# Performance work log

Measured on AMD Instinct MI355X. Metric: run time of the kernel, lower is better.

## Reference

```python
import jax, jax.numpy as jnp
import numpy as np

B, T, H, C, R = 8, 8192, 128, 128, 128  # batch, points, hidden, c_dim, plane reso
EPS = 1e-3  # 10e-4 in original
PLANE_COLS = ((0, 2), (0, 1), (1, 2))  # xz, xy, yz


def _normalize_coordinate(p, cols):
    # normalize_coordinate with padding=0.0: p in [-0.5,0.5] -> [0,1), clipped
    xy = p[..., jnp.array(cols)] / (1.0 + 0.0 + EPS) + 0.5
    return jnp.clip(xy, 0.0, 1.0 - EPS)


def _coordinate2index(xy):
    g = jnp.floor(xy * R).astype(jnp.int32)  # [B,T,2]
    return g[..., 0] + R * g[..., 1]  # [B,T]


def _resblock(x, w0, b0, w1, b1, ws):
    # ResnetBlockFC: fc_1(relu(fc_0(relu(x)))) + shortcut(x)
    net = jax.nn.relu(x) @ w0 + b0
    dx = jax.nn.relu(net) @ w1 + b1
    return x @ ws + dx


def _pool_local(c, idx_list):
    # c: [B,T,F]; scatter_max into R*R bins per plane, gather back, sum over planes
    def one(cb, ib):  # cb [T,F], ib [T]
        out = jnp.full((R * R, cb.shape[-1]), -jnp.inf, cb.dtype).at[ib].max(cb)
        out = jnp.where(jnp.isinf(out), jnp.zeros_like(out), out)  # empty bins -> 0
        return out[ib]  # gather-broadcast back to points
    pooled = jnp.zeros_like(c)
    for idx in idx_list:
        pooled = pooled + jax.vmap(one)(c, idx)
    return pooled


def _plane_features(cfeat, idx):
    # scatter_mean of [B,T,C] into [B, C, R, R]
    def one(cb, ib):  # cb [T,C], ib [T]
        sums = jnp.zeros((R * R, cb.shape[-1]), cb.dtype).at[ib].add(cb)
        cnt = jnp.zeros((R * R,), cb.dtype).at[ib].add(1.0)
        return sums / jnp.clip(cnt, 1.0, None)[:, None]
    m = jax.vmap(one)(cfeat, idx)  # [B, R*R, C]
    return m.transpose(0, 2, 1).reshape(cfeat.shape[0], cfeat.shape[-1], R, R)


def _forward(p, p2, wp, bp, wp2, bp2,
             blk_w0, blk_b0, blk_w1, blk_b1, blk_ws,
             blkc_w0, blkc_b0, blkc_w1, blkc_b1, blkc_ws,
             fc_c_w, fc_c_b, fc_cc_w, fc_cc_b):
    idx_list = [_coordinate2index(_normalize_coordinate(p, cols)) for cols in PLANE_COLS]

    # feat_pos (PointNetPlusPlusAttnFusion) surrogate: per-point projections + additive fusion
    net = p @ wp + bp                  # [B,T,2H] geometry stream
    net_corr = net + (p2 @ wp2 + bp2)  # [B,T,2H] fused articulation stream

    net = _resblock(net, blk_w0[0], blk_b0[0], blk_w1[0], blk_b1[0], blk_ws[0])
    for i in range(1, blk_w0.shape[0]):
        pooled = _pool_local(net, idx_list)
        net = _resblock(jnp.concatenate([net, pooled], axis=-1),
                        blk_w0[i], blk_b0[i], blk_w1[i], blk_b1[i], blk_ws[i])
    c = net @ fc_c_w + fc_c_b  # [B,T,C]

    net_corr = _resblock(net_corr, blkc_w0[0], blkc_b0[0], blkc_w1[0], blkc_b1[0], blkc_ws[0])
    for i in range(1, blkc_w0.shape[0]):
        pooled = _pool_local(net_corr, idx_list)
        net_corr = _resblock(jnp.concatenate([net_corr, pooled], axis=-1),
                             blkc_w0[i], blkc_b0[i], blkc_w1[i], blkc_b1[i], blkc_ws[i])
    c_corr = net_corr @ fc_cc_w + fc_cc_b  # [B,T,C]

    planes = [_plane_features(c, idx) for idx in idx_list]
    planes += [_plane_features(c_corr, idx) for idx in idx_list]
    # order: geo_xz, geo_xy, geo_yz, corr_xz, corr_xy, corr_yz
    return jnp.stack(planes)  # [6, B, C, R, R]


def setup_inputs() -> dict:
    key = jax.random.key(0)
    ks = jax.random.split(key, 24)
    s = 0.05
    def n(i, shape):
        return jax.random.normal(ks[i], shape, jnp.float32) * s
    NB = 5
    return {
        "p": jax.random.uniform(ks[0], (B, T, 3), jnp.float32, -0.5, 0.5),
        "p2": jax.random.uniform(ks[1], (B, T, 3), jnp.float32, -0.5, 0.5),
        "wp": n(2, (3, 2 * H)), "bp": jnp.zeros((2 * H,), jnp.float32),
        "wp2": n(3, (3, 2 * H)), "bp2": jnp.zeros((2 * H,), jnp.float32),
        "blk_w0": n(4, (NB, 2 * H, H)), "blk_b0": jnp.zeros((NB, H), jnp.float32),
        "blk_w1": n(5, (NB, H, H)), "blk_b1": jnp.zeros((NB, H), jnp.float32),
        "blk_ws": n(6, (NB, 2 * H, H)),
        "blkc_w0": n(7, (NB, 2 * H, H)), "blkc_b0": jnp.zeros((NB, H), jnp.float32),
        "blkc_w1": n(8, (NB, H, H)), "blkc_b1": jnp.zeros((NB, H), jnp.float32),
        "blkc_ws": n(9, (NB, 2 * H, H)),
        "fc_c_w": n(10, (H, C)), "fc_c_b": jnp.zeros((C,), jnp.float32),
        "fc_cc_w": n(11, (H, C)), "fc_cc_b": jnp.zeros((C,), jnp.float32),
    }


def reference(p, p2, wp, bp, wp2, bp2,
              blk_w0, blk_b0, blk_w1, blk_b1, blk_ws,
              blkc_w0, blkc_b0, blkc_w1, blkc_b1, blkc_ws,
              fc_c_w, fc_c_b, fc_cc_w, fc_cc_b):
    return _forward(p, p2, wp, bp, wp2, bp2,
                    blk_w0, blk_b0, blk_w1, blk_b1, blk_ws,
                    blkc_w0, blkc_b0, blkc_w1, blkc_b1, blkc_ws,
                    fc_c_w, fc_c_b, fc_cc_w, fc_cc_b)
```

## Files before the change

### kernel.cpp

```cpp
#include <hip/hip_runtime.h>
#include <cstdint>
#include <cstddef>

#define Bn 8
#define Tn 8192
#define BT (Bn*Tn)
#define Hn 128
#define RRn 16384

typedef unsigned short u16;
typedef __attribute__((ext_vector_type(8))) short s8v;
typedef __attribute__((ext_vector_type(4))) float f4v;

#define SSTR ((size_t)BT*128)

__device__ __forceinline__ u16 f2bf(float f) {
  unsigned u = __float_as_uint(f);
  unsigned r = (u + 0x7FFF + ((u >> 16) & 1)) >> 16;
  return (u16)r;
}
__device__ __forceinline__ unsigned pack2(float a, float b) {
  return (unsigned)f2bf(a) | ((unsigned)f2bf(b) << 16);
}

__device__ __forceinline__ s8v relu8(s8v a) {
  union { s8v s; unsigned u[4]; } x; x.s = a;
#pragma unroll
  for (int k = 0; k < 4; ++k) {
    unsigned m = ((x.u[k] & 0x80008000u) >> 15) * 0xFFFFu;
    x.u[k] &= ~m;
  }
  return x.s;
}

__device__ __forceinline__ void upk(unsigned u, float& lo, float& hi) {
  lo = __uint_as_float(u << 16);
  hi = __uint_as_float(u & 0xFFFF0000u);
}

__global__ void k_idx(const float* __restrict__ p, int* __restrict__ idx,
                      int* __restrict__ cnt32) {
  int i = blockIdx.x*256 + threadIdx.x;
  if (i >= BT) return;
  int b = i >> 13;
  float v0 = p[i*3+0], v1 = p[i*3+1], v2 = p[i*3+2];
  float v[3] = {v0, v1, v2};
  const int A0[3] = {0,0,1};
  const int A1[3] = {2,1,2};
#pragma unroll
  for (int pl = 0; pl < 3; ++pl) {
    float a = v[A0[pl]] / 1.001f + 0.5f;
    float bq = v[A1[pl]] / 1.001f + 0.5f;
    a = fminf(fmaxf(a, 0.0f), 0.999f);
    bq = fminf(fmaxf(bq, 0.0f), 0.999f);
    int ga = (int)floorf(a * 128.0f);
    int gb = (int)floorf(bq * 128.0f);
    int bin = ga + 128*gb;
    idx[pl*BT + i] = bin;
    atomicAdd(&cnt32[(pl*Bn + b)*RRn + bin], 1);
  }
}

__global__ void k_scan(const int* __restrict__ cnt32, int* __restrict__ starts,
                       int* __restrict__ cursor) {
  int seg = blockIdx.x;
  const int* c = cnt32 + seg*RRn;
  int* st = starts + seg*RRn;
  int* cu = cursor + seg*RRn;
  int t = threadIdx.x;
  __shared__ int part[256];
  int base = t*64;
  int sum = 0;
#pragma unroll 8
  for (int j = 0; j < 64; ++j) sum += c[base+j];
  part[t] = sum; __syncthreads();
  for (int ofs = 1; ofs < 256; ofs <<= 1) {
    int v = (t >= ofs) ? part[t-ofs] : 0;
    __syncthreads();
    part[t] += v;
    __syncthreads();
  }
  int run = (t ? part[t-1] : 0) + seg*Tn;
#pragma unroll 8
  for (int j = 0; j < 64; ++j) { st[base+j] = run; cu[base+j] = run; run += c[base+j]; }
}

__global__ void k_fill(const int* __restrict__ idx, int* __restrict__ cursor,
                       int* __restrict__ sorted) {
  int g = blockIdx.x*256 + threadIdx.x;
  if (g >= 3*BT) return;
  int pl = g >> 16, i = g & (BT-1);
  int b = i >> 13;
  int pos = atomicAdd(&cursor[(pl*Bn + b)*RRn + idx[g]], 1);
  sorted[pos] = i;
}

__global__ void k_prep(const float* __restrict__ bw0, const float* __restrict__ bw1,
                       const float* __restrict__ bws, const float* __restrict__ cw0,
                       const float* __restrict__ cw1, const float* __restrict__ cws,
                       const float* __restrict__ fcw, const float* __restrict__ fccw,
                       u16* __restrict__ arena) {
  int c = blockIdx.x;
  int s = c / 26, r = c % 26;
  const float* base;
  if (r < 10)      base = (s ? cw0 : bw0) + (size_t)(r >> 1)*32768 + (size_t)(r & 1)*16384;
  else if (r < 15) base = (s ? cw1 : bw1) + (size_t)(r - 10)*16384;
  else if (r < 25) base = (s ? cws : bws) + (size_t)((r - 15) >> 1)*32768 + (size_t)((r - 15) & 1)*16384;
  else             base = s ? fccw : fcw;
  __shared__ u16 ld[128*130];
#pragma unroll 4
  for (int it = 0; it < 64; ++it) {
    int lin = it*256 + threadIdx.x;
    int k = lin >> 7, n = lin & 127;
    ld[k*130 + n] = f2bf(base[lin]);
  }
  __syncthreads();
  u16* dst = arena + (size_t)c*16384;
#pragma unroll 4
  for (int it = 0; it < 64; ++it) {
    int lin = it*256 + threadIdx.x;
    int n = lin >> 7, k = lin & 127;
    dst[lin] = ld[k*130 + n];
  }
}

template<int MODE>
__global__ __launch_bounds__(512, 2) void k_rb(
    const u16* __restrict__ xAb, const u16* __restrict__ xBb,
    const float* __restrict__ p, const float* __restrict__ p2,
    const float* __restrict__ wp, const float* __restrict__ bp,
    const float* __restrict__ wp2, const float* __restrict__ bp2,
    const u16* __restrict__ arena,
    int cw00, int cw01, int cws0, int cws1, int cw1c, int cfcw,
    const float* __restrict__ b0g, const float* __restrict__ b0c,
    const float* __restrict__ b1g, const float* __restrict__ b1c,
    const float* __restrict__ fcbg, const float* __restrict__ fcbc,
    u16* __restrict__ outb)
{
  const int y = blockIdx.y;
  const u16* ar = arena + (size_t)y*26*16384;
  const u16* w00 = ar + (size_t)cw00*16384;
  const u16* w01 = ar + (size_t)cw01*16384;
  const u16* ws0 = ar + (size_t)cws0*16384;
  const u16* ws1 = ar + (size_t)cws1*16384;
  const u16* w1c = ar + (size_t)cw1c*16384;
  const u16* fcw = ar + (size_t)cfcw*16384;
  const float* b0 = y ? b0c : b0g;
  const float* b1 = y ? b1c : b1g;
  const float* fcb = y ? fcbc : fcbg;
  const u16* xA = xAb + (size_t)y*SSTR;
  const u16* xB = xBb + (size_t)y*SSTR;
  u16* outp = outb + (size_t)y*SSTR;

  __shared__ u16 xs [256*72];
  __shared__ u16 w0s[128*72];
  __shared__ u16 wss[128*72];
  __shared__ u16 hid[256*136];
  const int tid = threadIdx.x;
  const size_t row0 = (size_t)blockIdx.x * 256;
  const int l = tid & 63, w = tid >> 6;
  const int lm = l & 15, lg = l >> 4;
  const int trow = tid >> 1, th = tid & 1;
  const int wn = tid >> 2, wq = tid & 3;

  f4v acc_h[2][8], acc_s[2][8];
#pragma unroll
  for (int mi = 0; mi < 2; ++mi)
#pragma unroll
    for (int j = 0; j < 8; ++j) { acc_h[mi][j] = (f4v){0,0,0,0}; acc_s[mi][j] = (f4v){0,0,0,0}; }

  float pa0=0.f, pa1=0.f, pa2=0.f, pq0=0.f, pq1=0.f, pq2=0.f;
  if (MODE == 1) {
    int rr = (int)row0 + trow;
    pa0 = p[rr*3+0]; pa1 = p[rr*3+1]; pa2 = p[rr*3+2];
    if (y) { pq0 = p2[rr*3+0]; pq1 = p2[rr*3+1]; pq2 = p2[rr*3+2]; }
  }

  uint4 px0, px1, px2, px3, pwa, pwb, psa, psb;
  if (MODE != 1) {
    const uint4* s = (const uint4*)(xA + (row0 + trow)*128 + th*32);
    px0 = s[0]; px1 = s[1]; px2 = s[2]; px3 = s[3];
  }
  {
    const uint4* sw = (const uint4*)(w00 + wn*128 + wq*16);
    pwa = sw[0]; pwb = sw[1];
    const uint4* ss = (const uint4*)(ws0 + wn*128 + wq*16);
    psa = ss[0]; psb = ss[1];
  }

#pragma unroll 1
  for (int kc = 0; kc < 4; ++kc) {
    if (MODE == 1) {
      const int c0 = kc*64 + th*32;
      unsigned t16[16];
#pragma unroll
      for (int q = 0; q < 8; ++q) {
        int c = c0 + q*4;
        float4 w0v = *(const float4*)(wp + c);
        float4 w1v = *(const float4*)(wp + 256 + c);
        float4 w2v = *(const float4*)(wp + 512 + c);
        float4 bbv = *(const float4*)(bp + c);
        float v0 = pa0*w0v.x + pa1*w1v.x + pa2*w2v.x + bbv.x;
        float v1 = pa0*w0v.y + pa1*w1v.y + pa2*w2v.y + bbv.y;
        float v2 = pa0*w0v.z + pa1*w1v.z + pa2*w2v.z + bbv.z;
        float v3 = pa0*w0v.w + pa1*w1v.w + pa2*w2v.w + bbv.w;
        if (y) {
          float4 u0 = *(const float4*)(wp2 + c);
          float4 u1 = *(const float4*)(wp2 + 256 + c);
          float4 u2 = *(const float4*)(wp2 + 512 + c);
          float4 b2 = *(const float4*)(bp2 + c);
          v0 += pq0*u0.x + pq1*u1.x + pq2*u2.x + b2.x;
          v1 += pq0*u0.y + pq1*u1.y + pq2*u2.y + b2.y;
          v2 += pq0*u0.z + pq1*u1.z + pq2*u2.z + b2.z;
          v3 += pq0*u0.w + pq1*u1.w + pq2*u2.w + b2.w;
        }
        t16[q*2]   = pack2(v0, v1);
        t16[q*2+1] = pack2(v2, v3);
      }
      uint4* d = (uint4*)(xs + trow*72 + th*32);
      d[0] = make_uint4(t16[0], t16[1], t16[2], t16[3]);
      d[1] = make_uint4(t16[4], t16[5], t16[6], t16[7]);
      d[2] = make_uint4(t16[8], t16[9], t16[10], t16[11]);
      d[3] = make_uint4(t16[12], t16[13], t16[14], t16[15]);
    } else {
      uint4* d = (uint4*)(xs + trow*72 + th*32);
      d[0] = px0; d[1] = px1; d[2] = px2; d[3] = px3;
    }
    { uint4* d = (uint4*)(w0s + wn*72 + wq*16); d[0] = pwa; d[1] = pwb; }
    { uint4* d = (uint4*)(wss + wn*72 + wq*16); d[0] = psa; d[1] = psb; }
    __syncthreads();
    if (kc < 3) {
      const int kn = kc + 1;
      const int k0n = (kn & 1) * 64;
      if (MODE != 1) {
        const u16* xsrcn = (kn < 2) ? xA : xB;
        const uint4* s = (const uint4*)(xsrcn + (row0 + trow)*128 + k0n + th*32);
        px0 = s[0]; px1 = s[1]; px2 = s[2]; px3 = s[3];
      }
      const u16* w0srcn = (kn < 2) ? w00 : w01;
      const u16* wssrcn = (kn < 2) ? ws0 : ws1;
      const uint4* sw = (const uint4*)(w0srcn + wn*128 + k0n + wq*16);
      pwa = sw[0]; pwb = sw[1];
      const uint4* ss = (const uint4*)(wssrcn + wn*128 + k0n + wq*16);
      psa = ss[0]; psb = ss[1];
    }
#pragma unroll
    for (int kk = 0; kk < 2; ++kk) {
      const int ko = lg*8 + kk*32;
      s8v a0 = *(const s8v*)(xs + (w*32 + lm)*72 + ko);
      s8v a1 = *(const s8v*)(xs + (w*32 + 16 + lm)*72 + ko);
      s8v a0r = relu8(a0), a1r = relu8(a1);
#pragma unroll
      for (int nj = 0; nj < 8; ++nj) {
        s8v bh = *(const s8v*)(w0s + (nj*16 + lm)*72 + ko);
        acc_h[0][nj] = __builtin_amdgcn_mfma_f32_16x16x32_bf16(a0r, bh, acc_h[0][nj], 0, 0, 0);
        acc_h[1][nj] = __builtin_amdgcn_mfma_f32_16x16x32_bf16(a1r, bh, acc_h[1][nj], 0, 0, 0);
      }
#pragma unroll
      for (int nj = 0; nj < 8; ++nj) {
        s8v bs = *(const s8v*)(wss + (nj*16 + lm)*72 + ko);
        acc_s[0][nj] = __builtin_amdgcn_mfma_f32_16x16x32_bf16(a0, bs, acc_s[0][nj], 0, 0, 0);
        acc_s[1][nj] = __builtin_amdgcn_mfma_f32_16x16x32_bf16(a1, bs, acc_s[1][nj], 0, 0, 0);
      }
    }
    __syncthreads();
  }
  {
    const uint4* s1 = (const uint4*)(w1c + wn*128 + wq*16);
    uint4 aa = s1[0], bb2 = s1[1];
    const uint4* s2 = (const uint4*)(w1c + wn*128 + 64 + wq*16);
    uint4 cc = s2[0], dd = s2[1];
    { uint4* d = (uint4*)(w0s + wn*72 + wq*16); d[0] = aa; d[1] = bb2; }
    { uint4* d = (uint4*)(wss + wn*72 + wq*16); d[0] = cc; d[1] = dd; }
#pragma unroll
    for (int mi = 0; mi < 2; ++mi)
#pragma unroll
      for (int nj = 0; nj < 8; ++nj) {
        const int col = nj*16 + lm;
        const float bv = b0[col];
#pragma unroll
        for (int r = 0; r < 4; ++r) {
          int row = w*32 + mi*16 + lg*4 + r;
          hid[row*136 + col] = f2bf(fmaxf(acc_h[mi][nj][r] + bv, 0.0f));
        }
      }
  }
  __syncthreads();
#pragma unroll
  for (int kk = 0; kk < 4; ++kk) {
    const int koA = lg*8 + kk*32;
    const int koB = lg*8 + (kk & 1)*32;
    const u16* pb = (kk < 2) ? w0s : wss;
    s8v a0 = *(const s8v*)(hid + (w*32 + lm)*136 + koA);
    s8v a1 = *(const s8v*)(hid + (w*32 + 16 + lm)*136 + koA);
#pragma unroll
    for (int nj = 0; nj < 8; ++nj) {
      s8v bb = *(const s8v*)(pb + (nj*16 + lm)*72 + koB);
      acc_s[0][nj] = __builtin_amdgcn_mfma_f32_16x16x32_bf16(a0, bb, acc_s[0][nj], 0, 0, 0);
      acc_s[1][nj] = __builtin_amdgcn_mfma_f32_16x16x32_bf16(a1, bb, acc_s[1][nj], 0, 0, 0);
    }
  }
  if (MODE != 2) {
#pragma unroll
    for (int mi = 0; mi < 2; ++mi)
#pragma unroll
      for (int nj = 0; nj < 8; ++nj) {
        const int col = nj*16 + lm;
        const float bv = b1[col];
#pragma unroll
        for (int r = 0; r < 4; ++r) {
          int row = w*32 + mi*16 + lg*4 + r;
          outp[(row0 + row)*128 + col] = f2bf(acc_s[mi][nj][r] + bv);
        }
      }
  } else {
    __syncthreads();
    {
      const uint4* s1 = (const uint4*)(fcw + wn*128 + wq*16);
      uint4 aa = s1[0], bb2 = s1[1];
      const uint4* s2 = (const uint4*)(fcw + wn*128 + 64 + wq*16);
      uint4 cc = s2[0], dd = s2[1];
      { uint4* d = (uint4*)(w0s + wn*72 + wq*16); d[0] = aa; d[1] = bb2; }
      { uint4* d = (uint4*)(wss + wn*72 + wq*16); d[0] = cc; d[1] = dd; }
#pragma unroll
      for (int mi = 0; mi < 2; ++mi)
#pragma unroll
        for (int nj = 0; nj < 8; ++nj) {
          const int col = nj*16 + lm;
          const float bv = b1[col];
#pragma unroll
          for (int r = 0; r < 4; ++r) {
            int row = w*32 + mi*16 + lg*4 + r;
            hid[row*136 + col] = f2bf(acc_s[mi][nj][r] + bv);
          }
        }
    }
    __syncthreads();
    f4v accf[2][8];
#pragma unroll
    for (int mi = 0; mi < 2; ++mi)
#pragma unroll
      for (int j = 0; j < 8; ++j) accf[mi][j] = (f4v){0,0,0,0};
#pragma unroll
    for (int kk = 0; kk < 4; ++kk) {
      const int koA = lg*8 + kk*32;
      const int koB = lg*8 + (kk & 1)*32;
      const u16* pb = (kk < 2) ? w0s : wss;
      s8v a0 = *(const s8v*)(hid + (w*32 + lm)*136 + koA);
      s8v a1 = *(const s8v*)(hid + (w*32 + 16 + lm)*136 + koA);
#pragma unroll
      for (int nj = 0; nj < 8; ++nj) {
        s8v bb = *(const s8v*)(pb + (nj*16 + lm)*72 + koB);
        accf[0][nj] = __builtin_amdgcn_mfma_f32_16x16x32_bf16(a0, bb, accf[0][nj], 0, 0, 0);
        accf[1][nj] = __builtin_amdgcn_mfma_f32_16x16x32_bf16(a1, bb, accf[1][nj], 0, 0, 0);
      }
    }
#pragma unroll
    for (int mi = 0; mi < 2; ++mi)
#pragma unroll
      for (int nj = 0; nj < 8; ++nj) {
        const int col = nj*16 + lm;
        const float bv = fcb[col];
#pragma unroll
        for (int r = 0; r < 4; ++r) {
          int row = w*32 + mi*16 + lg*4 + r;
          outp[(row0 + row)*128 + col] = f2bf(accf[mi][nj][r] + bv);
        }
      }
  }
}

__global__ void k_pool(const int* __restrict__ idx, const int* __restrict__ starts,
                       const int* __restrict__ cnt32, const int* __restrict__ sorted,
                       const u16* __restrict__ netb, u16* __restrict__ pooledb) {
  const u16* net = netb + (size_t)blockIdx.y*SSTR;
  u16* pooled = pooledb + (size_t)blockIdx.y*SSTR;
  int g = blockIdx.x*256 + threadIdx.x;
  int sl = g & 15;
  int i = g >> 4;
  if (i >= BT) return;
  int b = i >> 13;
  float acc[8];
#pragma unroll
  for (int k = 0; k < 8; ++k) acc[k] = 0.0f;
#pragma unroll
  for (int pl = 0; pl < 3; ++pl) {
    int seg = (pl*Bn + b)*RRn + idx[pl*BT + i];
    int s = starts[seg];
    int e = s + cnt32[seg];
    float mx[8];
#pragma unroll
    for (int k = 0; k < 8; ++k) mx[k] = -3.0e38f;
    for (int j = s; j < e; ++j) {
      int jj = sorted[j];
      uint4 v = *(const uint4*)(net + (size_t)jj*128 + sl*8);
      float lo, hi;
      upk(v.x, lo, hi); mx[0] = fmaxf(mx[0], lo); mx[1] = fmaxf(mx[1], hi);
      upk(v.y, lo, hi); mx[2] = fmaxf(mx[2], lo); mx[3] = fmaxf(mx[3], hi);
      upk(v.z, lo, hi); mx[4] = fmaxf(mx[4], lo); mx[5] = fmaxf(mx[5], hi);
      upk(v.w, lo, hi); mx[6] = fmaxf(mx[6], lo); mx[7] = fmaxf(mx[7], hi);
    }
#pragma unroll
    for (int k = 0; k < 8; ++k) acc[k] += mx[k];
  }
  union { uint4 v; unsigned u[4]; } o;
#pragma unroll
  for (int k = 0; k < 4; ++k)
    o.u[k] = (unsigned)f2bf(acc[2*k]) | ((unsigned)f2bf(acc[2*k+1]) << 16);
  *(uint4*)(pooled + (size_t)i*128 + sl*8) = o.v;
}

__global__ __launch_bounds__(256) void k_mean(
    const int* __restrict__ starts, const int* __restrict__ cnt32,
    const int* __restrict__ sorted, const u16* __restrict__ cbufb,
    float* __restrict__ out) {
  int W = blockIdx.x*4 + (threadIdx.x >> 6);
  int half = blockIdx.y;
  int lane = threadIdx.x & 63;
  int grp = W & 255;
  int b = (W >> 8) & 7;
  int plq = W >> 11;
  int ss = plq / 3, pl = plq - 3*ss;
  int bin = grp*64 + lane;
  int seg = (pl*Bn + b)*RRn + bin;
  int c = cnt32[seg];
  int s0 = starts[seg];
  float inv = (c > 0) ? 1.0f/(float)c : 0.0f;
  const u16* cb = cbufb + (size_t)ss*SSTR;
  size_t obase = ((size_t)(plq*Bn + b)*Hn)*RRn + bin;
  float sum[64];
#pragma unroll
  for (int k = 0; k < 64; ++k) sum[k] = 0.f;
  for (int j = 0; j < c; ++j) {
    int jj = sorted[s0 + j];
    const uint4* r = (const uint4*)(cb + (size_t)jj*128 + half*64);
#pragma unroll
    for (int k = 0; k < 8; ++k) {
      uint4 q = r[k];
      float lo, hi;
      upk(q.x, lo, hi); sum[k*8+0] += lo; sum[k*8+1] += hi;
      upk(q.y, lo, hi); sum[k*8+2] += lo; sum[k*8+3] += hi;
      upk(q.z, lo, hi); sum[k*8+4] += lo; sum[k*8+5] += hi;
      upk(q.w, lo, hi); sum[k*8+6] += lo; sum[k*8+7] += hi;
    }
  }
#pragma unroll
  for (int k = 0; k < 64; ++k)
    out[obase + (size_t)(half*64 + k)*RRn] = sum[k]*inv;
}

extern "C" void kernel_launch(void* const* d_in, const int* in_sizes, int n_in,
                              void* d_out_v, int out_size, void* d_ws, size_t ws_size,
                              hipStream_t stream) {
  const float* p    = (const float*)d_in[0];
  const float* p2   = (const float*)d_in[1];
  const float* wp   = (const float*)d_in[2];
  const float* bp   = (const float*)d_in[3];
  const float* wp2  = (const float*)d_in[4];
  const float* bp2  = (const float*)d_in[5];
  const float* bw0  = (const float*)d_in[6];
  const float* bb0  = (const float*)d_in[7];
  const float* bw1  = (const float*)d_in[8];
  const float* bb1  = (const float*)d_in[9];
  const float* bws  = (const float*)d_in[10];
  const float* cw0  = (const float*)d_in[11];
  const float* cb0  = (const float*)d_in[12];
  const float* cw1  = (const float*)d_in[13];
  const float* cb1  = (const float*)d_in[14];
  const float* cws  = (const float*)d_in[15];
  const float* fcw  = (const float*)d_in[16];
  const float* fcb  = (const float*)d_in[17];
  const float* fccw = (const float*)d_in[18];
  const float* fccb = (const float*)d_in[19];
  float* out = (float*)d_out_v;

  size_t off = 0;
  auto alloc = [&](size_t bytes) -> char* {
    char* r = (char*)d_ws + off;
    off += (bytes + 255) & ~(size_t)255;
    return r;
  };
  int* idx    = (int*)alloc((size_t)3*BT*4);
  int* cnt32  = (int*)alloc((size_t)3*Bn*RRn*4);
  int* starts = (int*)alloc((size_t)3*Bn*RRn*4);
  int* cursor = (int*)alloc((size_t)3*Bn*RRn*4);
  int* sorted = (int*)alloc((size_t)3*BT*4);
  u16* arena  = (u16*)alloc((size_t)52*16384*2);
  u16* buf0   = (u16*)alloc(2*SSTR*2);
  u16* buf1   = (u16*)alloc(2*SSTR*2);
  u16* bufP   = (u16*)alloc(2*SSTR*2);
  u16* cbuf   = (u16*)alloc(2*SSTR*2);
  if (off > ws_size) return;

  hipMemsetAsync(cnt32, 0, (size_t)3*Bn*RRn*4, stream);
  k_prep<<<52, 256, 0, stream>>>(bw0, bw1, bws, cw0, cw1, cws, fcw, fccw, arena);
  k_idx <<<BT/256, 256, 0, stream>>>(p, idx, cnt32);
  k_scan<<<24, 256, 0, stream>>>(cnt32, starts, cursor);
  k_fill<<<(3*BT)/256, 256, 0, stream>>>(idx, cursor, sorted);

  k_rb<1><<<dim3(BT/256, 2), 512, 0, stream>>>(
      nullptr, nullptr, p, p2, wp, bp, wp2, bp2,
      arena, 0, 1, 15, 16, 10, 25,
      bb0, cb0, bb1, cb1, nullptr, nullptr, buf1);
  u16* net = buf1; u16* other = buf0;
  for (int blk = 1; blk < 4; ++blk) {
    k_pool<<<dim3((BT*16)/256, 2), 256, 0, stream>>>(idx, starts, cnt32, sorted, net, bufP);
    k_rb<0><<<dim3(BT/256, 2), 512, 0, stream>>>(
        net, bufP, nullptr, nullptr, nullptr, nullptr, nullptr, nullptr,
        arena, 2*blk, 2*blk+1, 15+2*blk, 16+2*blk, 10+blk, 25,
        bb0 + blk*128, cb0 + blk*128, bb1 + blk*128, cb1 + blk*128,
        nullptr, nullptr, other);
    u16* t = net; net = other; other = t;
  }
  k_pool<<<dim3((BT*16)/256, 2), 256, 0, stream>>>(idx, starts, cnt32, sorted, net, bufP);
  k_rb<2><<<dim3(BT/256, 2), 512, 0, stream>>>(
      net, bufP, nullptr, nullptr, nullptr, nullptr, nullptr, nullptr,
      arena, 8, 9, 23, 24, 14, 25,
      bb0 + 4*128, cb0 + 4*128, bb1 + 4*128, cb1 + 4*128, fcb, fccb, cbuf);

  k_mean<<<dim3(3072, 2), 256, 0, stream>>>(starts, cnt32, sorted, cbuf, out);
}
```

Measured before the change: 525.8 us.

## Halve k_rb row tile to 128 and alias xs/hid LDS for higher occupancy

The resblock kernel now processes 128 rows per block instead of 256, so each wave owns one 16-row MFMA tile and holds half as many accumulators. The x staging buffer and the hidden buffer share one LDS region, and launch bounds now request 4 blocks per CU. The aim is lower register and LDS use per block so more blocks fit on a CU and latency is hidden better. In exchange, each block reloads the full weight tiles for half as many rows, which doubles weight traffic per output row and halves MFMA reuse of each B fragment.

```diff
diff --git a/kernel.cpp b/kernel.cpp
--- a/kernel.cpp
+++ b/kernel.cpp
@@ -125,7 +125,7 @@
 }
 
 template<int MODE>
-__global__ __launch_bounds__(512, 2) void k_rb(
+__global__ __launch_bounds__(512, 4) void k_rb(
     const u16* __restrict__ xAb, const u16* __restrict__ xBb,
     const float* __restrict__ p, const float* __restrict__ p2,
     const float* __restrict__ wp, const float* __restrict__ bp,
@@ -152,22 +152,20 @@
   const u16* xB = xBb + (size_t)y*SSTR;
   u16* outp = outb + (size_t)y*SSTR;
 
-  __shared__ u16 xs [256*72];
+  __shared__ u16 uni[128*136];
   __shared__ u16 w0s[128*72];
   __shared__ u16 wss[128*72];
-  __shared__ u16 hid[256*136];
+  u16* xs  = uni;
+  u16* hid = uni;
   const int tid = threadIdx.x;
-  const size_t row0 = (size_t)blockIdx.x * 256;
+  const size_t row0 = (size_t)blockIdx.x * 128;
   const int l = tid & 63, w = tid >> 6;
   const int lm = l & 15, lg = l >> 4;
-  const int trow = tid >> 1, th = tid & 1;
-  const int wn = tid >> 2, wq = tid & 3;
-
-  f4v acc_h[2][8], acc_s[2][8];
-#pragma unroll
-  for (int mi = 0; mi < 2; ++mi)
-#pragma unroll
-    for (int j = 0; j < 8; ++j) { acc_h[mi][j] = (f4v){0,0,0,0}; acc_s[mi][j] = (f4v){0,0,0,0}; }
+  const int trow = tid >> 2, tq = tid & 3;
+
+  f4v acc_h[8], acc_s[8];
+#pragma unroll
+  for (int j = 0; j < 8; ++j) { acc_h[j] = (f4v){0,0,0,0}; acc_s[j] = (f4v){0,0,0,0}; }
 
   float pa0=0.f, pa1=0.f, pa2=0.f, pq0=0.f, pq1=0.f, pq2=0.f;
   if (MODE == 1) {
@@ -176,25 +174,25 @@
     if (y) { pq0 = p2[rr*3+0]; pq1 = p2[rr*3+1]; pq2 = p2[rr*3+2]; }
   }
 
-  uint4 px0, px1, px2, px3, pwa, pwb, psa, psb;
+  uint4 px0, px1, pwa, pwb, psa, psb;
   if (MODE != 1) {
-    const uint4* s = (const uint4*)(xA + (row0 + trow)*128 + th*32);
-    px0 = s[0]; px1 = s[1]; px2 = s[2]; px3 = s[3];
+    const uint4* s = (const uint4*)(xA + (row0 + trow)*128 + tq*16);
+    px0 = s[0]; px1 = s[1];
   }
   {
-    const uint4* sw = (const uint4*)(w00 + wn*128 + wq*16);
+    const uint4* sw = (const uint4*)(w00 + trow*128 + tq*16);
     pwa = sw[0]; pwb = sw[1];
-    const uint4* ss = (const uint4*)(ws0 + wn*128 + wq*16);
+    const uint4* ss = (const uint4*)(ws0 + trow*128 + tq*16);
     psa = ss[0]; psb = ss[1];
   }
 
 #pragma unroll 1
   for (int kc = 0; kc < 4; ++kc) {
     if (MODE == 1) {
-      const int c0 = kc*64 + th*32;
-      unsigned t16[16];
-#pragma unroll
-      for (int q = 0; q < 8; ++q) {
+      const int c0 = kc*64 + tq*16;
+      unsigned t8[8];
+#pragma unroll
+      for (int q = 0; q < 4; ++q) {
         int c = c0 + q*4;
         float4 w0v = *(const float4*)(wp + c);
         float4 w1v = *(const float4*)(wp + 256 + c);
@@ -214,76 +212,69 @@
           v2 += pq0*u0.z + pq1*u1.z + pq2*u2.z + b2.z;
           v3 += pq0*u0.w + pq1*u1.w + pq2*u2.w + b2.w;
         }
-        t16[q*2]   = pack2(v0, v1);
-        t16[q*2+1] = pack2(v2, v3);
-      }
-      uint4* d = (uint4*)(xs + trow*72 + th*32);
-      d[0] = make_uint4(t16[0], t16[1], t16[2], t16[3]);
-      d[1] = make_uint4(t16[4], t16[5], t16[6], t16[7]);
-      d[2] = make_uint4(t16[8], t16[9], t16[10], t16[11]);
-      d[3] = make_uint4(t16[12], t16[13], t16[14], t16[15]);
+        t8[q*2]   = pack2(v0, v1);
+        t8[q*2+1] = pack2(v2, v3);
+      }
+      uint4* d = (uint4*)(xs + trow*72 + tq*16);
+      d[0] = make_uint4(t8[0], t8[1], t8[2], t8[3]);
+      d[1] = make_uint4(t8[4], t8[5], t8[6], t8[7]);
     } else {
-      uint4* d = (uint4*)(xs + trow*72 + th*32);
-      d[0] = px0; d[1] = px1; d[2] = px2; d[3] = px3;
-    }
-    { uint4* d = (uint4*)(w0s + wn*72 + wq*16); d[0] = pwa; d[1] = pwb; }
-    { uint4* d = (uint4*)(wss + wn*72 + wq*16); d[0] = psa; d[1] = psb; }
+      uint4* d = (uint4*)(xs + trow*72 + tq*16);
+      d[0] = px0; d[1] = px1;
+    }
+    { uint4* d = (uint4*)(w0s + trow*72 + tq*16); d[0] = pwa; d[1] = pwb; }
+    { uint4* d = (uint4*)(wss + trow*72 + tq*16); d[0] = psa; d[1] = psb; }
     __syncthreads();
     if (kc < 3) {
       const int kn = kc + 1;
       const int k0n = (kn & 1) * 64;
       if (MODE != 1) {
         const u16* xsrcn = (kn < 2) ? xA : xB;
-        const uint4* s = (const uint4*)(xsrcn + (row0 + trow)*128 + k0n + th*32);
-        px0 = s[0]; px1 = s[1]; px2 = s[2]; px3 = s[3];
+        const uint4* s = (const uint4*)(xsrcn + (row0 + trow)*128 + k0n + tq*16);
+        px0 = s[0]; px1 = s[1];
       }
       const u16* w0srcn = (kn < 2) ? w00 : w01;
       const u16* wssrcn = (kn < 2) ? ws0 : ws1;
-      const uint4* sw = (const uint4*)(w0srcn + wn*128 + k0n + wq*16);
+      const uint4* sw = (const uint4*)(w0srcn + trow*128 + k0n + tq*16);
       pwa = sw[0]; pwb = sw[1];
-      const uint4* ss = (const uint4*)(wssrcn + wn*128 + k0n + wq*16);
+      const uint4* ss = (const uint4*)(wssrcn + trow*128 + k0n + tq*16);
       psa = ss[0]; psb = ss[1];
     }
 #pragma unroll
     for (int kk = 0; kk < 2; ++kk) {
       const int ko = lg*8 + kk*32;
-      s8v a0 = *(const s8v*)(xs + (w*32 + lm)*72 + ko);
-      s8v a1 = *(const s8v*)(xs + (w*32 + 16 + lm)*72 + ko);
-      s8v a0r = relu8(a0), a1r = relu8(a1);
+      s8v a0 = *(const s8v*)(xs + (w*16 + lm)*72 + ko);
+      s8v a0r = relu8(a0);
 #pragma unroll
       for (int nj = 0; nj < 8; ++nj) {
         s8v bh = *(const s8v*)(w0s + (nj*16 + lm)*72 + ko);
-        acc_h[0][nj] = __builtin_amdgcn_mfma_f32_16x16x32_bf16(a0r, bh, acc_h[0][nj], 0, 0, 0);
-        acc_h[1][nj] = __builtin_amdgcn_mfma_f32_16x16x32_bf16(a1r, bh, acc_h[1][nj], 0, 0, 0);
+        acc_h[nj] = __builtin_amdgcn_mfma_f32_16x16x32_bf16(a0r, bh, acc_h[nj], 0, 0, 0);
       }
 #pragma unroll
       for (int nj = 0; nj < 8; ++nj) {
         s8v bs = *(const s8v*)(wss + (nj*16 + lm)*72 + ko);
-        acc_s[0][nj] = __builtin_amdgcn_mfma_f32_16x16x32_bf16(a0, bs, acc_s[0][nj], 0, 0, 0);
-        acc_s[1][nj] = __builtin_amdgcn_mfma_f32_16x16x32_bf16(a1, bs, acc_s[1][nj], 0, 0, 0);
+        acc_s[nj] = __builtin_amdgcn_mfma_f32_16x16x32_bf16(a0, bs, acc_s[nj], 0, 0, 0);
       }
     }
     __syncthreads();
   }
   {
-    const uint4* s1 = (const uint4*)(w1c + wn*128 + wq*16);
+    const uint4* s1 = (const uint4*)(w1c + trow*128 + tq*16);
     uint4 aa = s1[0], bb2 = s1[1];
-    const uint4* s2 = (const uint4*)(w1c + wn*128 + 64 + wq*16);
+    const uint4* s2 = (const uint4*)(w1c + trow*128 + 64 + tq*16);
     uint4 cc = s2[0], dd = s2[1];
-    { uint4* d = (uint4*)(w0s + wn*72 + wq*16); d[0] = aa; d[1] = bb2; }
-    { uint4* d = (uint4*)(wss + wn*72 + wq*16); d[0] = cc; d[1] = dd; }
-#pragma unroll
-    for (int mi = 0; mi < 2; ++mi)
-#pragma unroll
-      for (int nj = 0; nj < 8; ++nj) {
-        const int col = nj*16 + lm;
-        const float bv = b0[col];
-#pragma unroll
-        for (int r = 0; r < 4; ++r) {
-          int row = w*32 + mi*16 + lg*4 + r;
-          hid[row*136 + col] = f2bf(fmaxf(acc_h[mi][nj][r] + bv, 0.0f));
-        }
-      }
+    { uint4* d = (uint4*)(w0s + trow*72 + tq*16); d[0] = aa; d[1] = bb2; }
+    { uint4* d = (uint4*)(wss + trow*72 + tq*16); d[0] = cc; d[1] = dd; }
+#pragma unroll
+    for (int nj = 0; nj < 8; ++nj) {
+      const int col = nj*16 + lm;
+      const float bv = b0[col];
+#pragma unroll
+      for (int r = 0; r < 4; ++r) {
+        int row = w*16 + lg*4 + r;
+        hid[row*136 + col] = f2bf(fmaxf(acc_h[nj][r] + bv, 0.0f));
+      }
+    }
   }
   __syncthreads();
 #pragma unroll
@@ -291,82 +282,69 @@
     const int koA = lg*8 + kk*32;
     const int koB = lg*8 + (kk & 1)*32;
     const u16* pb = (kk < 2) ? w0s : wss;
-    s8v a0 = *(const s8v*)(hid + (w*32 + lm)*136 + koA);
-    s8v a1 = *(const s8v*)(hid + (w*32 + 16 + lm)*136 + koA);
+    s8v a0 = *(const s8v*)(hid + (w*16 + lm)*136 + koA);
 #pragma unroll
     for (int nj = 0; nj < 8; ++nj) {
       s8v bb = *(const s8v*)(pb + (nj*16 + lm)*72 + koB);
-      acc_s[0][nj] = __builtin_amdgcn_mfma_f32_16x16x32_bf16(a0, bb, acc_s[0][nj], 0, 0, 0);
-      acc_s[1][nj] = __builtin_amdgcn_mfma_f32_16x16x32_bf16(a1, bb, acc_s[1][nj], 0, 0, 0);
+      acc_s[nj] = __builtin_amdgcn_mfma_f32_16x16x32_bf16(a0, bb, acc_s[nj], 0, 0, 0);
     }
   }
   if (MODE != 2) {
 #pragma unroll
-    for (int mi = 0; mi < 2; ++mi)
+    for (int nj = 0; nj < 8; ++nj) {
+      const int col = nj*16 + lm;
+      const float bv = b1[col];
+#pragma unroll
+      for (int r = 0; r < 4; ++r) {
+        int row = w*16 + lg*4 + r;
+        outp[(row0 + row)*128 + col] = f2bf(acc_s[nj][r] + bv);
+      }
+    }
+  } else {
+    __syncthreads();
+    {
+      const uint4* s1 = (const uint4*)(fcw + trow*128 + tq*16);
+      uint4 aa = s1[0], bb2 = s1[1];
+      const uint4* s2 = (const uint4*)(fcw + trow*128 + 64 + tq*16);
+      uint4 cc = s2[0], dd = s2[1];
+      { uint4* d = (uint4*)(w0s + trow*72 + tq*16); d[0] = aa; d[1] = bb2; }
+      { uint4* d = (uint4*)(wss + trow*72 + tq*16); d[0] = cc; d[1] = dd; }
 #pragma unroll
       for (int nj = 0; nj < 8; ++nj) {
         const int col = nj*16 + lm;
         const float bv = b1[col];
 #pragma unroll
         for (int r = 0; r < 4; ++r) {
-          int row = w*32 + mi*16 + lg*4 + r;
-          outp[(row0 + row)*128 + col] = f2bf(acc_s[mi][nj][r] + bv);
+          int row = w*16 + lg*4 + r;
+          hid[row*136 + col] = f2bf(acc_s[nj][r] + bv);
         }
       }
-  } else {
+    }
     __syncthreads();
-    {
-      const uint4* s1 = (const uint4*)(fcw + wn*128 + wq*16);
-      uint4 aa = s1[0], bb2 = s1[1];
-      const uint4* s2 = (const uint4*)(fcw + wn*128 + 64 + wq*16);
-      uint4 cc = s2[0], dd = s2[1];
-      { uint4* d = (uint4*)(w0s + wn*72 + wq*16); d[0] = aa; d[1] = bb2; }
-      { uint4* d = (uint4*)(wss + wn*72 + wq*16); d[0] = cc; d[1] = dd; }
-#pragma unroll
-      for (int mi = 0; mi < 2; ++mi)
-#pragma unroll
-        for (int nj = 0; nj < 8; ++nj) {
-          const int col = nj*16 + lm;
-          const float bv = b1[col];
-#pragma unroll
-          for (int r = 0; r < 4; ++r) {
-            int row = w*32 + mi*16 + lg*4 + r;
-            hid[row*136 + col] = f2bf(acc_s[mi][nj][r] + bv);
-          }
-        }
-    }
-    __syncthreads();
-    f4v accf[2][8];
-#pragma unroll
-    for (int mi = 0; mi < 2; ++mi)
-#pragma unroll
-      for (int j = 0; j < 8; ++j) accf[mi][j] = (f4v){0,0,0,0};
+#pragma unroll
+    for (int j = 0; j < 8; ++j) acc_h[j] = (f4v){0,0,0,0};
 #pragma unroll
     for (int kk = 0; kk < 4; ++kk) {
       const int koA = lg*8 + kk*32;
       const int koB = lg*8 + (kk & 1)*32;
       const u16* pb = (kk < 2) ? w0s : wss;
-      s8v a0 = *(const s8v*)(hid + (w*32 + lm)*136 + koA);
-      s8v a1 = *(const s8v*)(hid + (w*32 + 16 + lm)*136 + koA);
+      s8v a0 = *(const s8v*)(hid + (w*16 + lm)*136 + koA);
 #pragma unroll
       for (int nj = 0; nj < 8; ++nj) {
         s8v bb = *(const s8v*)(pb + (nj*16 + lm)*72 + koB);
-        accf[0][nj] = __builtin_amdgcn_mfma_f32_16x16x32_bf16(a0, bb, accf[0][nj], 0, 0, 0);
-        accf[1][nj] = __builtin_amdgcn_mfma_f32_16x16x32_bf16(a1, bb, accf[1][nj], 0, 0, 0);
-      }
-    }
-#pragma unroll
-    for (int mi = 0; mi < 2; ++mi)
-#pragma unroll
-      for (int nj = 0; nj < 8; ++nj) {
-        const int col = nj*16 + lm;
-        const float bv = fcb[col];
-#pragma unroll
-        for (int r = 0; r < 4; ++r) {
-          int row = w*32 + mi*16 + lg*4 + r;
-          outp[(row0 + row)*128 + col] = f2bf(accf[mi][nj][r] + bv);
-        }
-      }
+        acc_h[nj] = __builtin_amdgcn_mfma_f32_16x16x32_bf16(a0, bb, acc_h[nj], 0, 0, 0);
+      }
+    }
+#pragma unroll
+    for (int nj = 0; nj < 8; ++nj) {
+      const int col = nj*16 + lm;
+      const float bv = fcb[col];
+#pragma unroll
+      for (int r = 0; r < 4; ++r) {
+        int row = w*16 + lg*4 + r;
+        outp[(row0 + row)*128 + col] = f2bf(acc_h[nj][r] + bv);
+      }
+    }
   }
 }
 
@@ -498,14 +476,14 @@
   k_scan<<<24, 256, 0, stream>>>(cnt32, starts, cursor);
   k_fill<<<(3*BT)/256, 256, 0, stream>>>(idx, cursor, sorted);
 
-  k_rb<1><<<dim3(BT/256, 2), 512, 0, stream>>>(
+  k_rb<1><<<dim3(BT/128, 2), 512, 0, stream>>>(
       nullptr, nullptr, p, p2, wp, bp, wp2, bp2,
       arena, 0, 1, 15, 16, 10, 25,
       bb0, cb0, bb1, cb1, nullptr, nullptr, buf1);
   u16* net = buf1; u16* other = buf0;
   for (int blk = 1; blk < 4; ++blk) {
     k_pool<<<dim3((BT*16)/256, 2), 256, 0, stream>>>(idx, starts, cnt32, sorted, net, bufP);
-    k_rb<0><<<dim3(BT/256, 2), 512, 0, stream>>>(
+    k_rb<0><<<dim3(BT/128, 2), 512, 0, stream>>>(
         net, bufP, nullptr, nullptr, nullptr, nullptr, nullptr, nullptr,
         arena, 2*blk, 2*blk+1, 15+2*blk, 16+2*blk, 10+blk, 25,
         bb0 + blk*128, cb0 + blk*128, bb1 + blk*128, cb1 + blk*128,
@@ -513,7 +491,7 @@
     u16* t = net; net = other; other = t;
   }
   k_pool<<<dim3((BT*16)/256, 2), 256, 0, stream>>>(idx, starts, cnt32, sorted, net, bufP);
-  k_rb<2><<<dim3(BT/256, 2), 512, 0, stream>>>(
+  k_rb<2><<<dim3(BT/128, 2), 512, 0, stream>>>(
       net, bufP, nullptr, nullptr, nullptr, nullptr, nullptr, nullptr,
       arena, 8, 9, 23, 24, 14, 25,
       bb0 + 4*128, cb0 + 4*128, bb1 + 4*128, cb1 + 4*128, fcb, fccb, cbuf);
```

New measurement: 566.2 us. +7.7%, slower.
